# Kernel optimization log

Measured on AMD Instinct MI355X. Metric: run time of the kernel, lower is better.

Reference implementation:

```python
import jax, jax.numpy as jnp
import numpy as np

INPUT_DIM = 512
OUTPUT_DIM = 512
GRID_SIZE = 16
INPUT_MIN = -1.0
INPUT_RANGE = 2.0


def setup_inputs() -> dict:
    key = jax.random.key(0)
    k_x, k_mix = jax.random.split(key)
    x = jax.random.normal(k_x, (65536, INPUT_DIM), dtype=jnp.float32)
    # per-dim spline tables: bases init zeros, slopes init 0.1 (as in torch)
    bases = jnp.zeros((INPUT_DIM, GRID_SIZE), dtype=jnp.float32)
    slopes = jnp.full((INPUT_DIM, GRID_SIZE), 0.1, dtype=jnp.float32)
    mix = jax.random.normal(k_mix, (OUTPUT_DIM, INPUT_DIM), dtype=jnp.float32) * 0.01
    bias = jnp.zeros((OUTPUT_DIM,), dtype=jnp.float32)
    return {"x": x, "bases": bases, "slopes": slopes, "mix": mix, "bias": bias}


def reference(x, bases, slopes, mix, bias):
    # x: [B, D]; bases/slopes: [D, G]; mix: [O, D]; bias: [O]
    B, D = x.shape
    G = bases.shape[1]
    x_norm = jnp.clip((x - INPUT_MIN) / INPUT_RANGE, 0.0, 1.0 - 1e-6)
    idx = jnp.clip((x_norm * G).astype(jnp.int32), 0, G - 1)        # [B, D]
    x_local = x_norm * G - idx.astype(x.dtype)                       # fractional position in cell
    # gather per-dim table entries: flatten [D, G] and index with d*G + idx
    flat_idx = jnp.arange(D, dtype=jnp.int32)[None, :] * G + idx    # [B, D]
    base = bases.reshape(-1)[flat_idx]                               # [B, D]
    slope = slopes.reshape(-1)[flat_idx]                             # [B, D]
    spline_out = base + slope * x_local                              # [B, D]
    y = jnp.einsum('bd,od->bo', spline_out, mix) + bias              # [B, O]
    return y
```

## Files before the change

kernel.cpp:

```cpp
#include <hip/hip_runtime.h>


#define DIMK 512
#define DIMN 512

typedef unsigned short u16;
typedef unsigned int u32;
typedef __attribute__((ext_vector_type(8))) __bf16 bf16x8;
typedef __attribute__((ext_vector_type(4))) float f32x4;

__device__ __forceinline__ u32 bf16rne(float f) {
    u32 u = __float_as_uint(f);
    return (u + 0x7fffu + ((u >> 16) & 1u)) >> 16;
}

__global__ void prep_kernel(const float* __restrict__ mix,
                            u16* __restrict__ mixb) {
    int t = blockIdx.x * 256 + threadIdx.x;
    float4 v = reinterpret_cast<const float4*>(mix)[t];
    ushort4 o;
    o.x = (u16)bf16rne(v.x);
    o.y = (u16)bf16rne(v.y);
    o.z = (u16)bf16rne(v.z);
    o.w = (u16)bf16rne(v.w);
    reinterpret_cast<ushort4*>(mixb)[t] = o;
}

__global__ __launch_bounds__(512, 4) void kan_kernel(
    const float* __restrict__ x, const float* __restrict__ bases,
    const float* __restrict__ slopes, const u16* __restrict__ mixb,
    const float* __restrict__ bias, float* __restrict__ y) {
    __shared__ u32 s_tab[16 * DIMK];
    __shared__ __align__(16) u16 sA[2][128 * 32];
    __shared__ __align__(16) u16 sB[2][256 * 32];

    const int tid = threadIdx.x;
    const int lane = tid & 63;
    const int wid = tid >> 6;
    const int quad = lane >> 4;
    const int l15 = lane & 15;
    const int wave_m = wid >> 1;
    const int wave_n = wid & 1;
    const int swz = (blockIdx.x & 7) * 128 + (blockIdx.x >> 3);
    const int m0 = (swz >> 1) * 128;
    const int n0 = (swz & 1) * 256;

#pragma unroll
    for (int k = 0; k < 16; k++) {
        int i = tid + k * 512;
        int dim = i >> 4, g = i & 15;
        u32 p = bf16rne(bases[i]) | (bf16rne(slopes[i]) << 16);
        s_tab[g * DIMK + (dim ^ g)] = p;
    }

    const int ar = tid >> 2;
    const int akg = tid & 3;
    const int awchunk = (ar << 2) | (akg ^ ((ar >> 1) & 3));
    const float4* xrow =
        reinterpret_cast<const float4*>(x + (size_t)(m0 + ar) * DIMK) + akg * 2;

    f32x4 acc[2][8];
#pragma unroll
    for (int i = 0; i < 2; i++)
#pragma unroll
        for (int j = 0; j < 8; j++) acc[i][j] = (f32x4){0.f, 0.f, 0.f, 0.f};

    auto stage_a = [&](u16* sAb, float4 a, float4 b, int kt) {
        float xs[8] = {a.x, a.y, a.z, a.w, b.x, b.y, b.z, b.w};
        const int dbase = kt * 32 + akg * 8;
        u32 h[8];
#pragma unroll
        for (int j = 0; j < 8; j++) {
            float xn = fminf(fmaxf((xs[j] + 1.0f) * 0.5f, 0.0f), 0.999999f);
            float tt = xn * 16.0f;
            int idx = (int)tt;
            u32 p = s_tab[idx * DIMK + ((dbase + j) ^ idx)];
            float base = __uint_as_float(p << 16);
            float slope = __uint_as_float(p & 0xffff0000u);
            float sp = fmaf(slope, tt - (float)idx, base);
            h[j] = bf16rne(sp);
        }
        int4 pk = make_int4((int)(h[0] | (h[1] << 16)), (int)(h[2] | (h[3] << 16)),
                            (int)(h[4] | (h[5] << 16)), (int)(h[6] | (h[7] << 16)));
        *reinterpret_cast<int4*>(&sAb[awchunk * 8]) = pk;
    };
    auto stage_b = [&](u16* sBb, int kt) {
#pragma unroll
        for (int i = 0; i < 2; i++) {
            int grp = wid * 2 + i;
            int n = grp * 16 + (lane >> 2);
            int c = (lane & 3) ^ ((n >> 1) & 3);
            const u16* gsrc = mixb + (size_t)(n0 + n) * DIMK + kt * 32 + c * 8;
            __builtin_amdgcn_global_load_lds(
                (const __attribute__((address_space(1))) void*)gsrc,
                (__attribute__((address_space(3))) void*)(&sBb[grp * 512]),
                16, 0, 0);
        }
    };

    float4 p0 = xrow[0], p1 = xrow[1];
    __syncthreads();
    stage_b(&sB[0][0], 0);
    __builtin_amdgcn_sched_barrier(0);
    float4 xs0a = xrow[8], xs0b = xrow[9];
    __builtin_amdgcn_sched_barrier(0);
    stage_a(&sA[0][0], p0, p1, 0);
    __builtin_amdgcn_sched_barrier(0);
    asm volatile("s_waitcnt vmcnt(2) lgkmcnt(0)" ::: "memory");
    __builtin_amdgcn_sched_barrier(0);
    __builtin_amdgcn_s_barrier();

    for (int kt = 0; kt < 16; ++kt) {
        const int p = kt & 1;
        const int q = p ^ 1;
        const bool do_stage = (kt < 15);

        float4 xna = xs0a, xnb = xs0b;
        if (do_stage) {
            stage_b(&sB[q][0], kt + 1);
            __builtin_amdgcn_sched_barrier(0);
            const int ktn = ((kt + 2) & 15) * 8;
            xna = xrow[ktn];
            xnb = xrow[ktn + 1];
            __builtin_amdgcn_sched_barrier(0);
            stage_a(&sA[q][0], xs0a, xs0b, kt + 1);
        }

        const u16* sAc = &sA[p][0];
        const u16* sBc = &sB[p][0];
        bf16x8 afrag[2];
#pragma unroll
        for (int fm = 0; fm < 2; fm++) {
            int m_l = wave_m * 32 + fm * 16 + l15;
            int ci = (m_l << 2) | (quad ^ ((m_l >> 1) & 3));
            afrag[fm] = *reinterpret_cast<const bf16x8*>(&sAc[ci * 8]);
        }
        __builtin_amdgcn_s_setprio(1);
#pragma unroll
        for (int fn = 0; fn < 8; fn++) {
            int n_l = wave_n * 128 + fn * 16 + l15;
            int ci = (n_l << 2) | (quad ^ ((n_l >> 1) & 3));
            bf16x8 bfrag = *reinterpret_cast<const bf16x8*>(&sBc[ci * 8]);
#pragma unroll
            for (int fm = 0; fm < 2; fm++)
                acc[fm][fn] = __builtin_amdgcn_mfma_f32_16x16x32_bf16(
                    afrag[fm], bfrag, acc[fm][fn], 0, 0, 0);
        }
        __builtin_amdgcn_s_setprio(0);

        if (do_stage) {
            __builtin_amdgcn_sched_barrier(0);
            asm volatile("s_waitcnt vmcnt(2) lgkmcnt(0)" ::: "memory");
            __builtin_amdgcn_sched_barrier(0);
            __builtin_amdgcn_s_barrier();
        }
        xs0a = xna;
        xs0b = xnb;
    }

#pragma unroll
    for (int fn = 0; fn < 8; fn++) {
        int o = n0 + wave_n * 128 + fn * 16 + l15;
        float bv = bias[o];
#pragma unroll
        for (int fm = 0; fm < 2; fm++) {
            int row = m0 + wave_m * 32 + fm * 16 + quad * 4;
            float* yp = y + (size_t)row * DIMN + o;
#pragma unroll
            for (int j = 0; j < 4; j++)
                yp[(size_t)j * DIMN] = acc[fm][fn][j] + bv;
        }
    }
}

extern "C" void kernel_launch(void* const* d_in, const int* in_sizes, int n_in,
                              void* d_out, int out_size, void* d_ws, size_t ws_size,
                              hipStream_t stream) {
    const float* x = (const float*)d_in[0];
    const float* bases = (const float*)d_in[1];
    const float* slopes = (const float*)d_in[2];
    const float* mix = (const float*)d_in[3];
    const float* bias = (const float*)d_in[4];
    float* y = (float*)d_out;

    u16* mixb = (u16*)d_ws;

    hipLaunchKernelGGL(prep_kernel, dim3(256), dim3(256), 0, stream, mix, mixb);
    hipLaunchKernelGGL(kan_kernel, dim3(1024), dim3(512), 0, stream,
                       x, bases, slopes, mixb, bias, y);
}
```

Measured before the change: 266.9 us.

## Split spline evaluation into separate kernel feeding a pure bf16 GEMM

Unfuses the spline computation from the GEMM: a new spline kernel writes bf16 activations to a workspace buffer, and a simpler GEMM kernel loads both operands directly into LDS via global_load_lds. The aim is to take the per-tile spline ALU work and x re-reads (x was re-read by both N tiles) out of the GEMM's critical path. The cost is an extra 64MB write plus read round-trip through HBM. A fused fallback, now without the manual waitcnt/setprio scheduling, is kept for when the workspace is too small.

```diff
diff --git a/kernel.cpp b/kernel.cpp
--- a/kernel.cpp
+++ b/kernel.cpp
@@ -26,11 +26,48 @@
     reinterpret_cast<ushort4*>(mixb)[t] = o;
 }
 
-__global__ __launch_bounds__(512, 4) void kan_kernel(
+__global__ __launch_bounds__(256) void spline_kernel(
     const float* __restrict__ x, const float* __restrict__ bases,
-    const float* __restrict__ slopes, const u16* __restrict__ mixb,
+    const float* __restrict__ slopes, u16* __restrict__ s) {
+    __shared__ u32 s_tab[16 * DIMK];
+
+    const int tid = threadIdx.x;
+#pragma unroll
+    for (int k = 0; k < 32; k++) {
+        int i = tid + k * 256;
+        int dim = i >> 4, g = i & 15;
+        u32 p = bf16rne(bases[i]) | (bf16rne(slopes[i]) << 16);
+        s_tab[g * DIMK + (dim ^ g)] = p;
+    }
+    __syncthreads();
+
+    const int base = blockIdx.x * 256 + tid;
+#pragma unroll 2
+    for (int it = 0; it < 8; it++) {
+        int i = base + it * 524288;
+        const float4* xp = reinterpret_cast<const float4*>(x) + (size_t)i * 2;
+        float4 a = xp[0], b = xp[1];
+        const int d0 = (i & 63) << 3;
+        float xs[8] = {a.x, a.y, a.z, a.w, b.x, b.y, b.z, b.w};
+        bf16x8 r;
+#pragma unroll
+        for (int j = 0; j < 8; j++) {
+            float xn = fminf(fmaxf((xs[j] + 1.0f) * 0.5f, 0.0f), 0.999999f);
+            float tt = xn * 16.0f;
+            int idx = (int)tt;
+            u32 p = s_tab[idx * DIMK + ((d0 + j) ^ idx)];
+            float bs = __uint_as_float(p << 16);
+            float sl = __uint_as_float(p & 0xffff0000u);
+            float sp = fmaf(sl, tt - (float)idx, bs);
+            r[j] = (__bf16)sp;
+        }
+        reinterpret_cast<bf16x8*>(s)[i] = r;
+    }
+}
+
+__global__ __launch_bounds__(512, 4) void gemm_kernel(
+    const u16* __restrict__ s, const u16* __restrict__ mixb,
     const float* __restrict__ bias, float* __restrict__ y) {
-    __shared__ u32 s_tab[16 * DIMK];
     __shared__ __align__(16) u16 sA[2][128 * 32];
     __shared__ __align__(16) u16 sB[2][256 * 32];
 
@@ -45,6 +82,102 @@
     const int m0 = (swz >> 1) * 128;
     const int n0 = (swz & 1) * 256;
 
+    auto stage = [&](int q, int kt) {
+        {
+            int r = wid * 16 + (lane >> 2);
+            int c = (lane & 3) ^ ((r >> 1) & 3);
+            const u16* gsrc = s + (size_t)(m0 + r) * DIMK + kt * 32 + c * 8;
+            __builtin_amdgcn_global_load_lds(
+                (const __attribute__((address_space(1))) void*)gsrc,
+                (__attribute__((address_space(3))) void*)(&sA[q][wid * 512]),
+                16, 0, 0);
+        }
+#pragma unroll
+        for (int i = 0; i < 2; i++) {
+            int grp = wid * 2 + i;
+            int n = grp * 16 + (lane >> 2);
+            int c = (lane & 3) ^ ((n >> 1) & 3);
+            const u16* gsrc = mixb + (size_t)(n0 + n) * DIMK + kt * 32 + c * 8;
+            __builtin_amdgcn_global_load_lds(
+                (const __attribute__((address_space(1))) void*)gsrc,
+                (__attribute__((address_space(3))) void*)(&sB[q][grp * 512]),
+                16, 0, 0);
+        }
+    };
+
+    f32x4 acc[2][8];
+#pragma unroll
+    for (int i = 0; i < 2; i++)
+#pragma unroll
+        for (int j = 0; j < 8; j++) acc[i][j] = (f32x4){0.f, 0.f, 0.f, 0.f};
+
+    stage(0, 0);
+    __syncthreads();
+
+    for (int kt = 0; kt < 16; ++kt) {
+        const int p = kt & 1;
+        const int q = p ^ 1;
+        if (kt < 15) stage(q, kt + 1);
+
+        const u16* sAc = &sA[p][0];
+        const u16* sBc = &sB[p][0];
+        bf16x8 afrag[2];
+#pragma unroll
+        for (int fm = 0; fm < 2; fm++) {
+            int m_l = wave_m * 32 + fm * 16 + l15;
+            int ci = (m_l << 2) | (quad ^ ((m_l >> 1) & 3));
+            afrag[fm] = *reinterpret_cast<const bf16x8*>(&sAc[ci * 8]);
+        }
+        __builtin_amdgcn_s_setprio(1);
+#pragma unroll
+        for (int fn = 0; fn < 8; fn++) {
+            int n_l = wave_n * 128 + fn * 16 + l15;
+            int ci = (n_l << 2) | (quad ^ ((n_l >> 1) & 3));
+            bf16x8 bfrag = *reinterpret_cast<const bf16x8*>(&sBc[ci * 8]);
+#pragma unroll
+            for (int fm = 0; fm < 2; fm++)
+                acc[fm][fn] = __builtin_amdgcn_mfma_f32_16x16x32_bf16(
+                    afrag[fm], bfrag, acc[fm][fn], 0, 0, 0);
+        }
+        __builtin_amdgcn_s_setprio(0);
+
+        if (kt < 15) __syncthreads();
+    }
+
+#pragma unroll
+    for (int fn = 0; fn < 8; fn++) {
+        int o = n0 + wave_n * 128 + fn * 16 + l15;
+        float bv = bias[o];
+#pragma unroll
+        for (int fm = 0; fm < 2; fm++) {
+            int row = m0 + wave_m * 32 + fm * 16 + quad * 4;
+            float* yp = y + (size_t)row * DIMN + o;
+#pragma unroll
+            for (int j = 0; j < 4; j++)
+                yp[(size_t)j * DIMN] = acc[fm][fn][j] + bv;
+        }
+    }
+}
+
+__global__ __launch_bounds__(512, 4) void kan_fused_kernel(
+    const float* __restrict__ x, const float* __restrict__ bases,
+    const float* __restrict__ slopes, const u16* __restrict__ mixb,
+    const float* __restrict__ bias, float* __restrict__ y) {
+    __shared__ u32 s_tab[16 * DIMK];
+    __shared__ __align__(16) u16 sA[2][128 * 32];
+    __shared__ __align__(16) u16 sB[2][256 * 32];
+
+    const int tid = threadIdx.x;
+    const int lane = tid & 63;
+    const int wid = tid >> 6;
+    const int quad = lane >> 4;
+    const int l15 = lane & 15;
+    const int wave_m = wid >> 1;
+    const int wave_n = wid & 1;
+    const int swz = (blockIdx.x & 7) * 128 + (blockIdx.x >> 3);
+    const int m0 = (swz >> 1) * 128;
+    const int n0 = (swz & 1) * 256;
+
 #pragma unroll
     for (int k = 0; k < 16; k++) {
         int i = tid + k * 512;
@@ -75,9 +208,9 @@
             float tt = xn * 16.0f;
             int idx = (int)tt;
             u32 p = s_tab[idx * DIMK + ((dbase + j) ^ idx)];
-            float base = __uint_as_float(p << 16);
-            float slope = __uint_as_float(p & 0xffff0000u);
-            float sp = fmaf(slope, tt - (float)idx, base);
+            float bs = __uint_as_float(p << 16);
+            float sl = __uint_as_float(p & 0xffff0000u);
+            float sp = fmaf(sl, tt - (float)idx, bs);
             h[j] = bf16rne(sp);
         }
         int4 pk = make_int4((int)(h[0] | (h[1] << 16)), (int)(h[2] | (h[3] << 16)),
@@ -101,14 +234,9 @@
     float4 p0 = xrow[0], p1 = xrow[1];
     __syncthreads();
     stage_b(&sB[0][0], 0);
-    __builtin_amdgcn_sched_barrier(0);
     float4 xs0a = xrow[8], xs0b = xrow[9];
-    __builtin_amdgcn_sched_barrier(0);
     stage_a(&sA[0][0], p0, p1, 0);
-    __builtin_amdgcn_sched_barrier(0);
-    asm volatile("s_waitcnt vmcnt(2) lgkmcnt(0)" ::: "memory");
-    __builtin_amdgcn_sched_barrier(0);
-    __builtin_amdgcn_s_barrier();
+    __syncthreads();
 
     for (int kt = 0; kt < 16; ++kt) {
         const int p = kt & 1;
@@ -118,11 +246,9 @@
         float4 xna = xs0a, xnb = xs0b;
         if (do_stage) {
             stage_b(&sB[q][0], kt + 1);
-            __builtin_amdgcn_sched_barrier(0);
             const int ktn = ((kt + 2) & 15) * 8;
             xna = xrow[ktn];
             xnb = xrow[ktn + 1];
-            __builtin_amdgcn_sched_barrier(0);
             stage_a(&sA[q][0], xs0a, xs0b, kt + 1);
         }
 
@@ -135,7 +261,6 @@
             int ci = (m_l << 2) | (quad ^ ((m_l >> 1) & 3));
             afrag[fm] = *reinterpret_cast<const bf16x8*>(&sAc[ci * 8]);
         }
-        __builtin_amdgcn_s_setprio(1);
 #pragma unroll
         for (int fn = 0; fn < 8; fn++) {
             int n_l = wave_n * 128 + fn * 16 + l15;
@@ -146,14 +271,8 @@
                 acc[fm][fn] = __builtin_amdgcn_mfma_f32_16x16x32_bf16(
                     afrag[fm], bfrag, acc[fm][fn], 0, 0, 0);
         }
-        __builtin_amdgcn_s_setprio(0);
-
-        if (do_stage) {
-            __builtin_amdgcn_sched_barrier(0);
-            asm volatile("s_waitcnt vmcnt(2) lgkmcnt(0)" ::: "memory");
-            __builtin_amdgcn_sched_barrier(0);
-            __builtin_amdgcn_s_barrier();
-        }
+
+        if (do_stage) __syncthreads();
         xs0a = xna;
         xs0b = xnb;
     }
@@ -184,8 +303,18 @@
     float* y = (float*)d_out;
 
     u16* mixb = (u16*)d_ws;
+    const size_t NEED = 512 * 1024 + (size_t)65536 * 512 * 2;
 
     hipLaunchKernelGGL(prep_kernel, dim3(256), dim3(256), 0, stream, mix, mixb);
-    hipLaunchKernelGGL(kan_kernel, dim3(1024), dim3(512), 0, stream,
-                       x, bases, slopes, mixb, bias, y);
-}
+
+    if (ws_size >= NEED) {
+        u16* sbuf = mixb + 512 * 1024 / 2;
+        hipLaunchKernelGGL(spline_kernel, dim3(2048), dim3(256), 0, stream,
+                           x, bases, slopes, sbuf);
+        hipLaunchKernelGGL(gemm_kernel, dim3(1024), dim3(512), 0, stream,
+                           sbuf, mixb, bias, y);
+    } else {
+        hipLaunchKernelGGL(kan_fused_kernel, dim3(1024), dim3(512), 0, stream,
+                           x, bases, slopes, mixb, bias, y);
+    }
+}
```

Measured after the change: 289.1 us. +8.3%, slower.
